# Kernel tuning notes

Measured on AMD Instinct MI355X. Metric: run time of the kernel, lower is better.

## Reference

```python
import jax, jax.numpy as jnp
import numpy as np

N, CIN, COUT, K, S, H, W = 16, 512, 512, 3, 512, 64, 64
EPS = 1e-8


def setup_inputs() -> dict:
    key = jax.random.key(0)
    k1, k2, k3, k4 = jax.random.split(key, 4)
    return {
        "x": jax.random.normal(k1, (N, CIN, H, W), jnp.float32),
        "style": jax.random.normal(k2, (N, S), jnp.float32),
        # conv weight ~ N(0,1) as in the torch module (lr_mul=1)
        "weight": jax.random.normal(k3, (COUT, CIN, K, K), jnp.float32),
        # style modulation linear: weight ~ N(0,1), bias init 1.0
        "style_w": jax.random.normal(k4, (CIN, S), jnp.float32),
        "style_b": jnp.ones((CIN,), jnp.float32),
    }


def reference(x, style, weight, style_w, style_b):
    # equalized-lr scales (gain=1.0, lr_mul=1.0, mode=fan_in)
    lin_scale = 1.0 / jnp.sqrt(jnp.float32(S))          # fan_in of linear = style_channels
    w_scale = 1.0 / jnp.sqrt(jnp.float32(CIN * K * K))  # fan_in of weight[0] = Cin*k*k

    # style modulation: s[n, cin] (style_bias = 0.0)
    s = style @ (style_w.T * lin_scale) + style_b        # [N, Cin]

    w = weight * w_scale                                  # [Cout, Cin, K, K]

    # demodulation: rsqrt(sum_{i,kh,kw} (w[o,i]*s[n,i])^2 + eps) per (n, o)
    demod = jax.lax.rsqrt(jnp.einsum('oikl,ni->no', w * w, s * s) + EPS)  # [N, Cout]

    # fused form: conv(x * s, W) * demod  ==  grouped conv with per-sample modulated weights
    xs = x * s[:, :, None, None]
    out = jax.lax.conv_general_dilated(
        xs, w, window_strides=(1, 1), padding='SAME',
        dimension_numbers=('NCHW', 'OIHW', 'NCHW'))
    return out * demod[:, :, None, None]
```

## Files before the change

kernel.cpp:

```cpp
#include <hip/hip_runtime.h>
#include <hip/hip_bf16.h>

#define CIN   512
#define COUT  512
#define HW    4096
#define PADW  66
#define NB    16
#define KTOT  4608
#define BUFSZ 65536
#define BOFF  32768

static constexpr float LIN_SCALE = 0.044194173824159216f;
static constexpr float W_SCALE   = 0.014731391274719738f;

typedef __attribute__((ext_vector_type(8))) short bf16x8;
typedef __attribute__((ext_vector_type(4))) float f32x4;

__device__ __forceinline__ unsigned short f2us(float f) {
    __hip_bfloat16 h = __float2bfloat16(f); unsigned short u; __builtin_memcpy(&u, &h, 2); return u;
}

typedef const __attribute__((address_space(1))) unsigned int guint;
typedef __attribute__((address_space(3))) unsigned int luint;
__device__ __forceinline__ void gload_lds16(const void* g, void* l) {
    __builtin_amdgcn_global_load_lds((guint*)g, (luint*)l, 16, 0, 0);
}

__global__ void k_style(const float* __restrict__ style,
                        const float* __restrict__ style_w,
                        const float* __restrict__ style_b,
                        float* __restrict__ s) {
    int wid  = (blockIdx.x * blockDim.x + threadIdx.x) >> 6;
    int lane = threadIdx.x & 63;
    int n = wid >> 9, i = wid & 511;
    float sum = 0.f;
    for (int j = lane; j < 512; j += 64)
        sum += style[n * 512 + j] * style_w[i * 512 + j];
    for (int m = 32; m; m >>= 1) sum += __shfl_xor(sum, m, 64);
    if (lane == 0) s[n * 512 + i] = sum * LIN_SCALE + style_b[i];
}

__global__ void k_wprep(const float* __restrict__ weight,
                        float* __restrict__ wsq,
                        __hip_bfloat16* __restrict__ wt) {
    int oi = blockIdx.x * 256 + threadIdx.x;
    int o = oi >> 9, i = oi & 511;
    float sq = 0.f;
#pragma unroll
    for (int tp = 0; tp < 9; ++tp) {
        float v = weight[(size_t)oi * 9 + tp] * W_SCALE;
        sq += v * v;
        wt[(size_t)o * KTOT + tp * 512 + i] = __float2bfloat16(v);
    }
    wsq[oi] = sq;
}

__global__ void k_demod(const float* __restrict__ wsq, const float* __restrict__ s,
                        float* __restrict__ demod) {
    int wid  = (blockIdx.x * blockDim.x + threadIdx.x) >> 6;
    int lane = threadIdx.x & 63;
    int n = wid >> 9, o = wid & 511;
    float sum = 0.f;
    for (int i = lane; i < 512; i += 64) {
        float sv = s[n * 512 + i];
        sum += wsq[o * 512 + i] * sv * sv;
    }
    for (int m = 32; m; m >>= 1) sum += __shfl_xor(sum, m, 64);
    if (lane == 0) demod[n * 512 + o] = rsqrtf(sum + 1e-8f);
}

__global__ void k_border(__hip_bfloat16* __restrict__ xs) {
    int bp = blockIdx.x, n = blockIdx.y, t = threadIdx.x;
    int hp, wp;
    if (bp < 66)       { hp = 0;  wp = bp; }
    else if (bp < 132) { hp = 65; wp = bp - 66; }
    else { int k2 = bp - 132; hp = 1 + (k2 >> 1); wp = (k2 & 1) ? 65 : 0; }
    uint4 z = make_uint4(0u, 0u, 0u, 0u);
    *(uint4*)(xs + (((size_t)n * PADW * PADW) + hp * PADW + wp) * 512 + t * 8) = z;
}

__global__ void k_xs(const float* __restrict__ x, const float* __restrict__ s,
                     __hip_bfloat16* __restrict__ xs) {
    const int h = blockIdx.x;
    const int n = blockIdx.y;
    const int t = threadIdx.x;
    const int PITCH = 66;
    __shared__ float lds[64 * 66];
    for (int ic = 0; ic < 8; ++ic) {
        const int i0 = ic * 64;
        __syncthreads();
#pragma unroll
        for (int j = 0; j < 4; ++j) {
            int idx = j * 256 + t;
            int il = idx >> 4;
            int wq = (idx & 15) * 4;
            float4 v = *(const float4*)(x + (((size_t)n * 512 + i0 + il) * HW) + h * 64 + wq);
            float* dst = &lds[il * PITCH + wq];
            dst[0] = v.x; dst[1] = v.y; dst[2] = v.z; dst[3] = v.w;
        }
        __syncthreads();
#pragma unroll
        for (int j = 0; j < 2; ++j) {
            int idx = j * 256 + t;
            int wp = idx >> 3;
            int ib = (idx & 7) * 8;
            unsigned short tmp[8];
#pragma unroll
            for (int r = 0; r < 8; ++r) {
                float xv = lds[(ib + r) * PITCH + wp];
                float sv = s[n * 512 + i0 + ib + r];
                tmp[r] = f2us(xv * sv);
            }
            uint4 o;
            o.x = (unsigned)tmp[0] | ((unsigned)tmp[1] << 16);
            o.y = (unsigned)tmp[2] | ((unsigned)tmp[3] << 16);
            o.z = (unsigned)tmp[4] | ((unsigned)tmp[5] << 16);
            o.w = (unsigned)tmp[6] | ((unsigned)tmp[7] << 16);
            *(uint4*)(xs + ((size_t)((n * PADW + h + 1) * PADW + (wp + 1))) * 512 + i0 + ib) = o;
        }
    }
}

#define BAR      __builtin_amdgcn_s_barrier()
#define WAITLGKM asm volatile("s_waitcnt lgkmcnt(0)" ::: "memory")
#define LOAD_B(CH) { _Pragma("unroll") for (int t_ = 0; t_ < 4; ++t_) \
    bfr[t_] = *(const bf16x8*)(cb + BOFF + bRow + t_ * 2048 + (CH)); }
#define LOAD_A(MG, CH) { _Pragma("unroll") for (int t_ = 0; t_ < 4; ++t_) \
    af[t_] = *(const bf16x8*)(cb + aRow + ((MG) * 4 + t_) * 2048 + (CH)); }
#define DO_MFMA(MG) { __builtin_amdgcn_s_setprio(1); \
    _Pragma("unroll") for (int m_ = 0; m_ < 4; ++m_) \
    _Pragma("unroll") for (int n_ = 0; n_ < 4; ++n_) \
        acc[(MG) * 4 + m_][n_] = __builtin_amdgcn_mfma_f32_16x16x32_bf16( \
            af[m_], bfr[n_], acc[(MG) * 4 + m_][n_], 0, 0, 0); \
    __builtin_amdgcn_s_setprio(0); }

__global__ __launch_bounds__(512, 2) void k_conv(
        const __hip_bfloat16* __restrict__ wt,
        const __hip_bfloat16* __restrict__ xs,
        const float* __restrict__ demod,
        float* __restrict__ out) {
    __shared__ __attribute__((aligned(16))) char smem[2 * BUFSZ];
    const int tid  = threadIdx.x;
    const int wv   = tid >> 6, lane = tid & 63;
    const int wm   = wv >> 2,  wn   = wv & 3;

    const int bid = blockIdx.x;
    const int xcd = bid & 7, idx = bid >> 3;
    const int pT  = idx & 15;
    const int o0  = ((idx >> 4) & 1) * 256;
    const int smp = xcd * 2 + (idx >> 5);

    const __hip_bfloat16* xsn = xs + (size_t)smp * (PADW * PADW * 512);

    const int rw = lane >> 3, cl = lane & 7;
    const int lc = cl ^ rw;
    const size_t aOff = (size_t)(wv * 8 + rw) * KTOT + lc * 8;
    const size_t bOff = (size_t)(wv * 8 + rw) * 512  + lc * 8;
    const __hip_bfloat16* aStage = wt  + (size_t)o0 * KTOT + aOff;
    const __hip_bfloat16* bStage = xsn + bOff;

    const int col = lane & 15, qd = lane >> 4;
    const int ch0 = ((qd)     ^ (col & 7)) << 4;
    const int ch1 = ((qd + 4) ^ (col & 7)) << 4;
    const int aRow = (wm * 128 + col) * 128;
    const int bRow = (wn * 64  + col) * 128;

    f32x4 acc[8][4] = {};

    {
        char* nbB = smem + BOFF + wv * 1024;
        char* nbA = smem + wv * 1024;
        const __hip_bfloat16* bS = bStage + (size_t)(pT * 4) * 33792;
        gload_lds16(bS,              nbB);
        gload_lds16(bS + 33792,      nbB + 8192);
        gload_lds16(bS + 2 * 33792,  nbB + 2 * 8192);
        gload_lds16(bS + 3 * 33792,  nbB + 3 * 8192);
        gload_lds16(aStage,              nbA);
        gload_lds16(aStage + 2 * 294912, nbA + 2 * 8192);
        gload_lds16(aStage + 294912,     nbA + 8192);
        gload_lds16(aStage + 3 * 294912, nbA + 3 * 8192);
        asm volatile("s_waitcnt vmcnt(2)" ::: "memory");
        BAR;
    }

    for (int kt = 0; kt < 71; ++kt) {
        char* cb = smem + (kt & 1) * BUFSZ;
        char* nb = smem + ((kt + 1) & 1) * BUFSZ;
        const int kt1  = kt + 1;
        const int tap1 = kt1 >> 3, c1 = kt1 & 7;
        const int kh1  = tap1 / 3, kw1 = tap1 - kh1 * 3;
        const __hip_bfloat16* aS = aStage + (size_t)kt1 * 64;
        const __hip_bfloat16* bS = bStage +
            (size_t)((pT * 4 + kh1) * PADW + kw1) * 512 + c1 * 64;
        char* nbB = nb + BOFF + wv * 1024;
        char* nbA = nb + wv * 1024;

        bf16x8 af[4], bfr[4];

        LOAD_B(ch0); LOAD_A(0, ch0);
        gload_lds16(bS,             nbB);
        gload_lds16(bS + 33792,     nbB + 8192);
        gload_lds16(bS + 2 * 33792, nbB + 2 * 8192);
        BAR; WAITLGKM;
        DO_MFMA(0);
        asm volatile("s_waitcnt vmcnt(3)" ::: "memory");
        BAR;

        LOAD_A(1, ch0);
        gload_lds16(bS + 3 * 33792, nbB + 3 * 8192);
        gload_lds16(aS,             nbA);
        gload_lds16(aS + 2 * 294912, nbA + 2 * 8192);
        BAR; WAITLGKM;
        DO_MFMA(1);
        BAR;

        LOAD_B(ch1); LOAD_A(0, ch1);
        gload_lds16(aS + 294912,     nbA + 8192);
        gload_lds16(aS + 3 * 294912, nbA + 3 * 8192);
        BAR; WAITLGKM;
        DO_MFMA(0);
        BAR;

        LOAD_A(1, ch1);
        BAR; WAITLGKM;
        DO_MFMA(1);
        asm volatile("s_waitcnt vmcnt(2)" ::: "memory");
        BAR;
    }

    {
        char* cb = smem + BUFSZ;
        asm volatile("s_waitcnt vmcnt(0)" ::: "memory");
        BAR;
        bf16x8 af[4], bfr[4];
        LOAD_B(ch0); LOAD_A(0, ch0); DO_MFMA(0);
        LOAD_A(1, ch0);              DO_MFMA(1);
        LOAD_B(ch1); LOAD_A(0, ch1); DO_MFMA(0);
        LOAD_A(1, ch1);              DO_MFMA(1);
    }

    const int hwBase = pT * 256 + wn * 64 + col;
#pragma unroll
    for (int m = 0; m < 8; ++m) {
#pragma unroll
        for (int rg = 0; rg < 4; ++rg) {
            const int o = o0 + wm * 128 + m * 16 + qd * 4 + rg;
            const float dm = demod[smp * 512 + o];
            float* orow = out + ((size_t)(smp * COUT + o)) * HW + hwBase;
#pragma unroll
            for (int nn = 0; nn < 4; ++nn)
                orow[nn * 16] = acc[m][nn][rg] * dm;
        }
    }
}

extern "C" void kernel_launch(void* const* d_in, const int* in_sizes, int n_in,
                              void* d_out, int out_size, void* d_ws, size_t ws_size,
                              hipStream_t stream) {
    const float* x       = (const float*)d_in[0];
    const float* style   = (const float*)d_in[1];
    const float* weight  = (const float*)d_in[2];
    const float* style_w = (const float*)d_in[3];
    const float* style_b = (const float*)d_in[4];
    float* out = (float*)d_out;

    char* ws = (char*)d_ws;
    float*          s_buf  = (float*)(ws + 0);
    float*          wsq    = (float*)(ws + 32768);
    float*          demod  = (float*)(ws + 1081344);
    __hip_bfloat16* wt     = (__hip_bfloat16*)(ws + 1114112);
    __hip_bfloat16* xs     = (__hip_bfloat16*)(ws + 5832704);

    k_style <<<dim3(2048),     dim3(256), 0, stream>>>(style, style_w, style_b, s_buf);
    k_wprep <<<dim3(1024),     dim3(256), 0, stream>>>(weight, wsq, wt);
    k_demod <<<dim3(2048),     dim3(256), 0, stream>>>(wsq, s_buf, demod);
    k_border<<<dim3(260, 16),  dim3(64),  0, stream>>>(xs);
    k_xs    <<<dim3(64, 16),   dim3(256), 0, stream>>>(x, s_buf, xs);
    k_conv  <<<dim3(512),      dim3(512), 0, stream>>>(wt, xs, demod, out);
}
```

Before: 503.3 us.

## Fuse prep kernels and compute demodulation inside the conv epilogue

Merges the style and weight-prep kernels into one launch, folds the border zeroing into the xs kernel, and computes the demodulation factors in the conv kernel's epilogue from wsq and s, which removes the separate demod kernel. Six launches become three, cutting launch overhead and inter-kernel gaps. The xs kernel now handles two rows per block, uses an LDS pitch of 65 to reduce bank conflicts, and caches s in shared memory. The trade-off is that each conv block recomputes 256 dot products of length 512 after its main loop, and this epilogue is not overlapped with compute.

```diff
diff --git a/kernel.cpp b/kernel.cpp
--- a/kernel.cpp
+++ b/kernel.cpp
@@ -26,90 +26,84 @@
     __builtin_amdgcn_global_load_lds((guint*)g, (luint*)l, 16, 0, 0);
 }
 
-__global__ void k_style(const float* __restrict__ style,
-                        const float* __restrict__ style_w,
-                        const float* __restrict__ style_b,
-                        float* __restrict__ s) {
-    int wid  = (blockIdx.x * blockDim.x + threadIdx.x) >> 6;
-    int lane = threadIdx.x & 63;
-    int n = wid >> 9, i = wid & 511;
-    float sum = 0.f;
-    for (int j = lane; j < 512; j += 64)
-        sum += style[n * 512 + j] * style_w[i * 512 + j];
-    for (int m = 32; m; m >>= 1) sum += __shfl_xor(sum, m, 64);
-    if (lane == 0) s[n * 512 + i] = sum * LIN_SCALE + style_b[i];
-}
-
-__global__ void k_wprep(const float* __restrict__ weight,
-                        float* __restrict__ wsq,
-                        __hip_bfloat16* __restrict__ wt) {
-    int oi = blockIdx.x * 256 + threadIdx.x;
-    int o = oi >> 9, i = oi & 511;
-    float sq = 0.f;
-#pragma unroll
-    for (int tp = 0; tp < 9; ++tp) {
-        float v = weight[(size_t)oi * 9 + tp] * W_SCALE;
-        sq += v * v;
-        wt[(size_t)o * KTOT + tp * 512 + i] = __float2bfloat16(v);
-    }
-    wsq[oi] = sq;
-}
-
-__global__ void k_demod(const float* __restrict__ wsq, const float* __restrict__ s,
-                        float* __restrict__ demod) {
-    int wid  = (blockIdx.x * blockDim.x + threadIdx.x) >> 6;
-    int lane = threadIdx.x & 63;
-    int n = wid >> 9, o = wid & 511;
-    float sum = 0.f;
-    for (int i = lane; i < 512; i += 64) {
-        float sv = s[n * 512 + i];
-        sum += wsq[o * 512 + i] * sv * sv;
-    }
-    for (int m = 32; m; m >>= 1) sum += __shfl_xor(sum, m, 64);
-    if (lane == 0) demod[n * 512 + o] = rsqrtf(sum + 1e-8f);
-}
-
-__global__ void k_border(__hip_bfloat16* __restrict__ xs) {
-    int bp = blockIdx.x, n = blockIdx.y, t = threadIdx.x;
-    int hp, wp;
-    if (bp < 66)       { hp = 0;  wp = bp; }
-    else if (bp < 132) { hp = 65; wp = bp - 66; }
-    else { int k2 = bp - 132; hp = 1 + (k2 >> 1); wp = (k2 & 1) ? 65 : 0; }
-    uint4 z = make_uint4(0u, 0u, 0u, 0u);
-    *(uint4*)(xs + (((size_t)n * PADW * PADW) + hp * PADW + wp) * 512 + t * 8) = z;
+__global__ void k_prep(const float* __restrict__ weight,
+                       const float* __restrict__ style,
+                       const float* __restrict__ style_w,
+                       const float* __restrict__ style_b,
+                       float* __restrict__ wsq,
+                       __hip_bfloat16* __restrict__ wt,
+                       float* __restrict__ s) {
+    const int bid = blockIdx.x;
+    if (bid < 1024) {
+        int oi = bid * 256 + threadIdx.x;
+        int o = oi >> 9, i = oi & 511;
+        float sq = 0.f;
+#pragma unroll
+        for (int tp = 0; tp < 9; ++tp) {
+            float v = weight[(size_t)oi * 9 + tp] * W_SCALE;
+            sq += v * v;
+            wt[(size_t)o * KTOT + tp * 512 + i] = __float2bfloat16(v);
+        }
+        wsq[oi] = sq;
+    } else {
+        int wid  = (bid - 1024) * 4 + (threadIdx.x >> 6);
+        int lane = threadIdx.x & 63;
+        int n = wid >> 9, i = wid & 511;
+        float sum = 0.f;
+        for (int j = lane; j < 512; j += 64)
+            sum += style[n * 512 + j] * style_w[i * 512 + j];
+        for (int m = 32; m; m >>= 1) sum += __shfl_xor(sum, m, 64);
+        if (lane == 0) s[n * 512 + i] = sum * LIN_SCALE + style_b[i];
+    }
 }
 
 __global__ void k_xs(const float* __restrict__ x, const float* __restrict__ s,
                      __hip_bfloat16* __restrict__ xs) {
-    const int h = blockIdx.x;
     const int n = blockIdx.y;
     const int t = threadIdx.x;
-    const int PITCH = 66;
-    __shared__ float lds[64 * 66];
+    if (blockIdx.x == 32) {
+        uint4 z = make_uint4(0u, 0u, 0u, 0u);
+        for (int idx = t; idx < 16640; idx += 512) {
+            int bp = idx >> 6, sl = idx & 63;
+            int hp, wp;
+            if (bp < 66)       { hp = 0;  wp = bp; }
+            else if (bp < 132) { hp = 65; wp = bp - 66; }
+            else { int k2 = bp - 132; hp = 1 + (k2 >> 1); wp = (k2 & 1) ? 65 : 0; }
+            *(uint4*)(xs + (((size_t)n * PADW * PADW) + hp * PADW + wp) * 512 + sl * 8) = z;
+        }
+        return;
+    }
+    const int half = t >> 8;
+    const int tt   = t & 255;
+    const int h    = blockIdx.x * 2 + half;
+    const int PITCH = 65;
+    __shared__ float lds[2][64 * 65];
+    __shared__ float sv[512];
+    float* ld = lds[half];
+    sv[t] = s[n * 512 + t];
     for (int ic = 0; ic < 8; ++ic) {
         const int i0 = ic * 64;
         __syncthreads();
 #pragma unroll
         for (int j = 0; j < 4; ++j) {
-            int idx = j * 256 + t;
+            int idx = j * 256 + tt;
             int il = idx >> 4;
             int wq = (idx & 15) * 4;
             float4 v = *(const float4*)(x + (((size_t)n * 512 + i0 + il) * HW) + h * 64 + wq);
-            float* dst = &lds[il * PITCH + wq];
+            float* dst = &ld[il * PITCH + wq];
             dst[0] = v.x; dst[1] = v.y; dst[2] = v.z; dst[3] = v.w;
         }
         __syncthreads();
 #pragma unroll
         for (int j = 0; j < 2; ++j) {
-            int idx = j * 256 + t;
+            int idx = j * 256 + tt;
             int wp = idx >> 3;
             int ib = (idx & 7) * 8;
             unsigned short tmp[8];
 #pragma unroll
             for (int r = 0; r < 8; ++r) {
-                float xv = lds[(ib + r) * PITCH + wp];
-                float sv = s[n * 512 + i0 + ib + r];
-                tmp[r] = f2us(xv * sv);
+                float xv = ld[(ib + r) * PITCH + wp];
+                tmp[r] = f2us(xv * sv[i0 + ib + r]);
             }
             uint4 o;
             o.x = (unsigned)tmp[0] | ((unsigned)tmp[1] << 16);
@@ -137,7 +131,8 @@
 __global__ __launch_bounds__(512, 2) void k_conv(
         const __hip_bfloat16* __restrict__ wt,
         const __hip_bfloat16* __restrict__ xs,
-        const float* __restrict__ demod,
+        const float* __restrict__ wsq,
+        const float* __restrict__ s_buf,
         float* __restrict__ out) {
     __shared__ __attribute__((aligned(16))) char smem[2 * BUFSZ];
     const int tid  = threadIdx.x;
@@ -184,11 +179,12 @@
     }
 
     for (int kt = 0; kt < 71; ++kt) {
-        char* cb = smem + (kt & 1) * BUFSZ;
-        char* nb = smem + ((kt + 1) & 1) * BUFSZ;
+        const char* cb = smem + (kt & 1) * BUFSZ;
+        char* nb = (char*)smem + ((kt + 1) & 1) * BUFSZ;
         const int kt1  = kt + 1;
         const int tap1 = kt1 >> 3, c1 = kt1 & 7;
-        const int kh1  = tap1 / 3, kw1 = tap1 - kh1 * 3;
+        const int kh1  = (tap1 * 11) >> 5;
+        const int kw1  = tap1 - kh1 * 3;
         const __hip_bfloat16* aS = aStage + (size_t)kt1 * 64;
         const __hip_bfloat16* bS = bStage +
             (size_t)((pT * 4 + kh1) * PADW + kw1) * 512 + c1 * 64;
@@ -229,7 +225,7 @@
     }
 
     {
-        char* cb = smem + BUFSZ;
+        const char* cb = smem + BUFSZ;
         asm volatile("s_waitcnt vmcnt(0)" ::: "memory");
         BAR;
         bf16x8 af[4], bfr[4];
@@ -239,13 +235,34 @@
         LOAD_A(1, ch1);              DO_MFMA(1);
     }
 
+    __syncthreads();
+    float* s2  = (float*)smem;
+    float* dml = (float*)(smem + 2048);
+    {
+        float sv = s_buf[smp * 512 + tid];
+        s2[tid] = sv * sv;
+    }
+    __syncthreads();
+#pragma unroll 4
+    for (int ow = 0; ow < 32; ++ow) {
+        const int o = wv * 32 + ow;
+        const float* wrow = wsq + (size_t)(o0 + o) * 512;
+        float sum = 0.f;
+#pragma unroll
+        for (int ii = 0; ii < 8; ++ii)
+            sum += wrow[ii * 64 + lane] * s2[ii * 64 + lane];
+        for (int m = 32; m; m >>= 1) sum += __shfl_xor(sum, m, 64);
+        if (lane == 0) dml[o] = rsqrtf(sum + 1e-8f);
+    }
+    __syncthreads();
+
     const int hwBase = pT * 256 + wn * 64 + col;
 #pragma unroll
     for (int m = 0; m < 8; ++m) {
 #pragma unroll
         for (int rg = 0; rg < 4; ++rg) {
             const int o = o0 + wm * 128 + m * 16 + qd * 4 + rg;
-            const float dm = demod[smp * 512 + o];
+            const float dm = dml[wm * 128 + m * 16 + qd * 4 + rg];
             float* orow = out + ((size_t)(smp * COUT + o)) * HW + hwBase;
 #pragma unroll
             for (int nn = 0; nn < 4; ++nn)
@@ -267,14 +284,11 @@
     char* ws = (char*)d_ws;
     float*          s_buf  = (float*)(ws + 0);
     float*          wsq    = (float*)(ws + 32768);
-    float*          demod  = (float*)(ws + 1081344);
     __hip_bfloat16* wt     = (__hip_bfloat16*)(ws + 1114112);
     __hip_bfloat16* xs     = (__hip_bfloat16*)(ws + 5832704);
 
-    k_style <<<dim3(2048),     dim3(256), 0, stream>>>(style, style_w, style_b, s_buf);
-    k_wprep <<<dim3(1024),     dim3(256), 0, stream>>>(weight, wsq, wt);
-    k_demod <<<dim3(2048),     dim3(256), 0, stream>>>(wsq, s_buf, demod);
-    k_border<<<dim3(260, 16),  dim3(64),  0, stream>>>(xs);
-    k_xs    <<<dim3(64, 16),   dim3(256), 0, stream>>>(x, s_buf, xs);
-    k_conv  <<<dim3(512),      dim3(512), 0, stream>>>(wt, xs, demod, out);
-}
+    k_prep <<<dim3(3072),    dim3(256), 0, stream>>>(weight, style, style_w, style_b,
+                                                     wsq, wt, s_buf);
+    k_xs   <<<dim3(33, 16),  dim3(512), 0, stream>>>(x, s_buf, xs);
+    k_conv <<<dim3(512),     dim3(512), 0, stream>>>(wt, xs, wsq, s_buf, out);
+}
```

New measurement: 521.0 us. 1.04x slower.
